# Kernel tuning notes

Measured on AMD Instinct MI355X. Metric: run time of the kernel, lower is better.

## Reference

```python
import jax, jax.numpy as jnp
import numpy as np


def setup_inputs() -> dict:
    key = jax.random.key(0)
    k1, k2 = jax.random.split(key)
    B, L, D = 2048, 512, 256
    x = jax.random.normal(k1, (B, L, D), dtype=jnp.float32)
    N = jax.random.randint(k2, (B,), 0, L, dtype=jnp.int64)
    N = jnp.maximum(N, 1)  # lengths must be >= 1
    return {"x": x, "N": N}


def reference(x, N):
    # Mean over the first N[b] elements along the sequence dim (keepdim=False).
    B, L, D = x.shape
    mask = (jnp.arange(L)[None, :] < N[:, None])  # [B, L]
    s = jnp.einsum('bld,bl->bd', x, mask.astype(x.dtype))  # masked sum
    return s / N[:, None].astype(x.dtype)  # [B, D]
```

## Files before the change

### kernel.cpp

```cpp
#include <hip/hip_runtime.h>


constexpr int LL = 512;
constexpr int DD = 256;
constexpr int D4 = DD / 4;
constexpr int LWAVES = 4;

__global__ __launch_bounds__(256) void capped_mean_kernel(
    const float* __restrict__ x,
    const int* __restrict__ N,
    float* __restrict__ out) {
  const int b    = blockIdx.x;
  const int tid  = threadIdx.x;
  const int d4   = tid & (D4 - 1);
  const int lrow = tid >> 6;

  const int n = N[b];

  const float4* __restrict__ x4 =
      reinterpret_cast<const float4*>(x + (size_t)b * LL * DD);

  float4 acc = make_float4(0.f, 0.f, 0.f, 0.f);

  #pragma unroll 4
  for (int l = lrow; l < n; l += LWAVES) {
    float4 v = x4[(size_t)l * D4 + d4];
    acc.x += v.x;
    acc.y += v.y;
    acc.z += v.z;
    acc.w += v.w;
  }

  __shared__ float4 red[LWAVES][D4];
  red[lrow][d4] = acc;
  __syncthreads();

  if (tid < D4) {
    float4 a0 = red[0][tid];
    float4 a1 = red[1][tid];
    float4 a2 = red[2][tid];
    float4 a3 = red[3][tid];
    const float inv = 1.0f / (float)n;
    float4 r;
    r.x = (a0.x + a1.x + a2.x + a3.x) * inv;
    r.y = (a0.y + a1.y + a2.y + a3.y) * inv;
    r.z = (a0.z + a1.z + a2.z + a3.z) * inv;
    r.w = (a0.w + a1.w + a2.w + a3.w) * inv;
    reinterpret_cast<float4*>(out)[(size_t)b * D4 + tid] = r;
  }
}

extern "C" void kernel_launch(void* const* d_in, const int* in_sizes, int n_in,
                              void* d_out, int out_size, void* d_ws, size_t ws_size,
                              hipStream_t stream) {
  const float* x = (const float*)d_in[0];
  const int*   N = (const int*)d_in[1];
  float*     out = (float*)d_out;

  const int B = in_sizes[1];

  dim3 grid(B);
  dim3 block(LWAVES * 64);
  hipLaunchKernelGGL(capped_mean_kernel, grid, block, 0, stream, x, N, out);
}
```

Baseline: 1.254 ms.

## Split sequence into chunks across blocks with a second reduction kernel

Each batch row's sequence is split into 64-row chunks, with one block per (batch, chunk) writing partial sums to the workspace. A second small kernel adds up the partials and divides by N. This spreads the uneven per-row work across many more blocks, which should improve load balance and the number of memory requests in flight. The cost is an extra kernel launch plus a write and re-read of the partial sums, and many blocks exit immediately when their chunk lies past N.

```diff
diff --git a/kernel.cpp b/kernel.cpp
--- a/kernel.cpp
+++ b/kernel.cpp
@@ -4,26 +4,30 @@
 constexpr int LL = 512;
 constexpr int DD = 256;
 constexpr int D4 = DD / 4;
-constexpr int LWAVES = 4;
+constexpr int CH = 64;
+constexpr int NCHUNK = LL / CH;
 
-__global__ __launch_bounds__(256) void capped_mean_kernel(
+__global__ __launch_bounds__(256) void capped_mean_partial(
     const float* __restrict__ x,
     const int* __restrict__ N,
-    float* __restrict__ out) {
-  const int b    = blockIdx.x;
-  const int tid  = threadIdx.x;
-  const int d4   = tid & (D4 - 1);
-  const int lrow = tid >> 6;
+    float4* __restrict__ part) {
+  const int b = blockIdx.x;
+  const int t = blockIdx.y;
+  const int n = N[b];
+  const int l0 = t * CH;
+  if (l0 >= n) return;
 
-  const int n = N[b];
+  const int lend = (l0 + CH < n) ? (l0 + CH) : n;
+  const int tid = threadIdx.x;
+  const int d4  = tid & (D4 - 1);
+  const int wl  = tid >> 6;
 
   const float4* __restrict__ x4 =
       reinterpret_cast<const float4*>(x + (size_t)b * LL * DD);
 
   float4 acc = make_float4(0.f, 0.f, 0.f, 0.f);
-
   #pragma unroll 4
-  for (int l = lrow; l < n; l += LWAVES) {
+  for (int l = l0 + wl; l < lend; l += 4) {
     float4 v = x4[(size_t)l * D4 + d4];
     acc.x += v.x;
     acc.y += v.y;
@@ -31,8 +35,8 @@
     acc.w += v.w;
   }
 
-  __shared__ float4 red[LWAVES][D4];
-  red[lrow][d4] = acc;
+  __shared__ float4 red[4][D4];
+  red[wl][d4] = acc;
   __syncthreads();
 
   if (tid < D4) {
@@ -40,14 +44,39 @@
     float4 a1 = red[1][tid];
     float4 a2 = red[2][tid];
     float4 a3 = red[3][tid];
-    const float inv = 1.0f / (float)n;
     float4 r;
-    r.x = (a0.x + a1.x + a2.x + a3.x) * inv;
-    r.y = (a0.y + a1.y + a2.y + a3.y) * inv;
-    r.z = (a0.z + a1.z + a2.z + a3.z) * inv;
-    r.w = (a0.w + a1.w + a2.w + a3.w) * inv;
-    reinterpret_cast<float4*>(out)[(size_t)b * D4 + tid] = r;
+    r.x = a0.x + a1.x + a2.x + a3.x;
+    r.y = a0.y + a1.y + a2.y + a3.y;
+    r.z = a0.z + a1.z + a2.z + a3.z;
+    r.w = a0.w + a1.w + a2.w + a3.w;
+    part[((size_t)b * NCHUNK + t) * D4 + tid] = r;
   }
+}
+
+__global__ __launch_bounds__(64) void capped_mean_final(
+    const float4* __restrict__ part,
+    const int* __restrict__ N,
+    float4* __restrict__ out) {
+  const int b   = blockIdx.x;
+  const int tid = threadIdx.x;
+  const int n   = N[b];
+  const int nt  = (n + CH - 1) / CH;
+
+  float4 s = make_float4(0.f, 0.f, 0.f, 0.f);
+  for (int t = 0; t < nt; ++t) {
+    float4 v = part[((size_t)b * NCHUNK + t) * D4 + tid];
+    s.x += v.x;
+    s.y += v.y;
+    s.z += v.z;
+    s.w += v.w;
+  }
+  const float inv = 1.0f / (float)n;
+  float4 r;
+  r.x = s.x * inv;
+  r.y = s.y * inv;
+  r.z = s.z * inv;
+  r.w = s.w * inv;
+  out[(size_t)b * D4 + tid] = r;
 }
 
 extern "C" void kernel_launch(void* const* d_in, const int* in_sizes, int n_in,
@@ -56,10 +85,14 @@
   const float* x = (const float*)d_in[0];
   const int*   N = (const int*)d_in[1];
   float*     out = (float*)d_out;
+  float4*   part = (float4*)d_ws;
 
   const int B = in_sizes[1];
 
-  dim3 grid(B);
-  dim3 block(LWAVES * 64);
-  hipLaunchKernelGGL(capped_mean_kernel, grid, block, 0, stream, x, N, out);
+  dim3 grid1(B, NCHUNK);
+  hipLaunchKernelGGL(capped_mean_partial, grid1, dim3(256), 0, stream, x, N, part);
+
+  dim3 grid2(B);
+  hipLaunchKernelGGL(capped_mean_final, grid2, dim3(64), 0, stream,
+                     (const float4*)part, N, (float4*)out);
 }
```

After: 1.241 ms. Within noise of the previous version (-1.0%).
